# Optimization experiments

Measured on AMD Instinct MI355X. Metric: run time of the kernel, lower is better.

The kernel has to match this reference:

```python
import jax, jax.numpy as jnp
import numpy as np

B, S, EMB, H = 2, 2048, 1024, 16
D = EMB // H  # per-head dim = 64
SCALE = 1.0 / np.sqrt(D).astype(np.float32)


def setup_inputs() -> dict:
    key = jax.random.key(0)
    ks = jax.random.split(key, 11)
    lim = 1.0 / np.sqrt(EMB).astype(np.float32)  # torch Linear default init range
    def lin(kw, kb):
        W = jax.random.uniform(kw, (EMB, EMB), jnp.float32, -lim, lim)
        b = jax.random.uniform(kb, (EMB,), jnp.float32, -lim, lim)
        return W, b
    Wq, bq = lin(ks[0], ks[1])
    Wk, bk = lin(ks[2], ks[3])
    Wv, bv = lin(ks[4], ks[5])
    Wo, bo = lin(ks[6], ks[7])
    xq = jax.random.normal(ks[8], (B, S, EMB), jnp.float32)
    xk = jax.random.normal(ks[9], (B, S, EMB), jnp.float32)
    xv = jax.random.normal(ks[10], (B, S, EMB), jnp.float32)
    mask = jnp.tril(jnp.ones((S, S), dtype=jnp.int32))  # causal mask; 0 -> blocked
    return {"xq": xq, "xk": xk, "xv": xv, "mask": mask,
            "Wq": Wq, "bq": bq, "Wk": Wk, "bk": bk,
            "Wv": Wv, "bv": bv, "Wo": Wo, "bo": bo}


def reference(xq, xk, xv, mask, Wq, bq, Wk, bk, Wv, bv, Wo, bo):
    # Projections (torch Linear: x @ W.T + b), then split heads: [B,S,E] -> [B,H,S,D]
    def split_heads(x):
        return x.reshape(B, S, H, D).transpose(0, 2, 1, 3)
    Q = split_heads(xq @ Wq.T + bq)
    K = split_heads(xk @ Wk.T + bk)
    V = split_heads(xv @ Wv.T + bv)
    scores = jnp.einsum("bhqd,bhkd->bhqk", Q, K) * SCALE  # [B,H,S,S]
    scores = jnp.where(mask[None, None, :, :] == 0, jnp.float32(-1e9), scores)
    attn = jax.nn.softmax(scores, axis=-1)  # softmax over key axis (dim=2 per-head in torch)
    res = jnp.einsum("bhqk,bhkd->bhqd", attn, V)
    res = res.transpose(0, 2, 1, 3).reshape(B, S, EMB)  # merge heads back (same slicing layout)
    return res @ Wo.T + bo
```

## Files before the change

### kernel.cpp

```cpp
#include <hip/hip_runtime.h>
#include <hip/hip_bf16.h>

#define BB   2
#define SS   2048
#define EMBD 1024
#define NH   16
#define HD   64
#define SCALE 0.125f
#define NEG_BIG (-1e30f)

typedef __bf16 bf16;
typedef float  floatx4 __attribute__((ext_vector_type(4)));
typedef __bf16 bf16x4  __attribute__((ext_vector_type(4)));
typedef __bf16 bf16x8  __attribute__((ext_vector_type(8)));

typedef const __attribute__((address_space(1))) void* gas_ptr;
typedef __attribute__((address_space(3))) void*       las_ptr;

__device__ __forceinline__ void gl_lds16(const void* g, void* l) {
    __builtin_amdgcn_global_load_lds((gas_ptr)g, (las_ptr)l, 16, 0, 0);
}

__global__ __launch_bounds__(256) void cvt_all(
    const float* __restrict__ xq, const float* __restrict__ xk,
    const float* __restrict__ xv, const float* __restrict__ Wq,
    const float* __restrict__ Wk, const float* __restrict__ Wv,
    const float* __restrict__ Wo, bf16* __restrict__ xqo,
    bf16* __restrict__ xko, bf16* __restrict__ xvo, bf16* __restrict__ Wqo,
    bf16* __restrict__ Wko, bf16* __restrict__ Wvo, bf16* __restrict__ Woo) {
    const int y = blockIdx.y;
    const float* src;
    bf16* dst;
    size_t n;
    const size_t NX = (size_t)BB * SS * EMBD;
    const size_t NW = (size_t)EMBD * EMBD;
    switch (y) {
        case 0: src = xq; dst = xqo; n = NX; break;
        case 1: src = xk; dst = xko; n = NX; break;
        case 2: src = xv; dst = xvo; n = NX; break;
        case 3: src = Wq; dst = Wqo; n = NW; break;
        case 4: src = Wk; dst = Wko; n = NW; break;
        case 5: src = Wv; dst = Wvo; n = NW; break;
        default: src = Wo; dst = Woo; n = NW; break;
    }
    const size_t stride = (size_t)gridDim.x * blockDim.x * 4;
    for (size_t i = ((size_t)blockIdx.x * blockDim.x + threadIdx.x) * 4;
         i < n; i += stride) {
        floatx4 v = *(const floatx4*)(src + i);
        bf16x4 o = {(bf16)v[0], (bf16)v[1], (bf16)v[2], (bf16)v[3]};
        *(bf16x4*)(dst + i) = o;
    }
}

template <int MODE>
__device__ __forceinline__ void gemm_body(const bf16* __restrict__ A,
                                          const bf16* __restrict__ W,
                                          const float* __restrict__ bias,
                                          void* __restrict__ Ov,
                                          int mBase, int nBase) {
    __shared__ __align__(16) bf16 As[2 * 128 * 32];
    __shared__ __align__(16) bf16 Bs[2 * 128 * 32];

    const int t = threadIdx.x;
    const int l = t & 63, w = t >> 6;
    const int lm = l & 15, lq = l >> 4;
    const int K = 1024;
    const int wm = (w >> 1) * 64, wn = (w & 1) * 64;

    const floatx4 zero = {0.f, 0.f, 0.f, 0.f};
    floatx4 acc[4][4];
#pragma unroll
    for (int i = 0; i < 4; i++)
#pragma unroll
        for (int j = 0; j < 4; j++) acc[i][j] = zero;

    for (int kb = 0; kb < K; kb += 64) {
        __syncthreads();
#pragma unroll
        for (int i = 0; i < 4; i++) {
            int half = i >> 1;
            int rem  = (i & 1) * 256 + t;
            int row  = rem >> 2;
            int col  = half * 32 + (rem & 3) * 8;
            const bf16* ga = A + (size_t)(mBase + row) * K + kb + col;
            const bf16* gb = W + (size_t)(nBase + row) * K + kb + col;
            char* la = (char*)As + (i * 256 + w * 64) * 16;
            char* lb = (char*)Bs + (i * 256 + w * 64) * 16;
            gl_lds16(ga, la);
            gl_lds16(gb, lb);
        }
        __syncthreads();

#pragma unroll
        for (int half = 0; half < 2; half++) {
            const bf16* Ah = As + half * 128 * 32;
            const bf16* Bh = Bs + half * 128 * 32;
            bf16x8 af[4], bfv[4];
#pragma unroll
            for (int f = 0; f < 4; f++) {
                int rowA = wm + f * 16 + lm;
                af[f] = *(const bf16x8*)&Ah[rowA * 32 + lq * 8];
                int rowB = wn + f * 16 + lm;
                bfv[f] = *(const bf16x8*)&Bh[rowB * 32 + lq * 8];
            }
            if (MODE == 2) {
#pragma unroll
                for (int i = 0; i < 4; i++)
#pragma unroll
                    for (int j = 0; j < 4; j++)
                        acc[i][j] = __builtin_amdgcn_mfma_f32_16x16x32_bf16(
                            bfv[i], af[j], acc[i][j], 0, 0, 0);
            } else {
#pragma unroll
                for (int fm = 0; fm < 4; fm++)
#pragma unroll
                    for (int fn = 0; fn < 4; fn++)
                        acc[fm][fn] =
                            __builtin_amdgcn_mfma_f32_16x16x32_bf16(
                                af[fm], bfv[fn], acc[fm][fn], 0, 0, 0);
            }
        }
    }

    if (MODE == 2) {
#pragma unroll
        for (int i = 0; i < 4; i++)
#pragma unroll
            for (int j = 0; j < 4; j++) {
                int m = mBase + wm + j * 16 + lm;
                int b = m >> 11, s = m & 2047;
#pragma unroll
                for (int r = 0; r < 4; r++) {
                    int n = nBase + wn + i * 16 + lq * 4 + r;
                    int h = n >> 6, d = n & 63;
                    float v = acc[i][j][r] + bias[n];
                    ((bf16*)Ov)[((size_t)(b * NH + h) * HD + d) * SS + s] =
                        (bf16)v;
                }
            }
    } else {
#pragma unroll
        for (int fn = 0; fn < 4; fn++) {
            int n = nBase + wn + fn * 16 + lm;
            float bv = bias[n];
#pragma unroll
            for (int fm = 0; fm < 4; fm++) {
                int m0 = mBase + wm + fm * 16 + lq * 4;
#pragma unroll
                for (int r = 0; r < 4; r++) {
                    int m = m0 + r;
                    float v = acc[fm][fn][r] + bv;
                    if (MODE == 0) {
                        int b = m >> 11, s = m & 2047;
                        int h = n >> 6, d = n & 63;
                        ((bf16*)Ov)[(((size_t)(b * NH + h)) * SS + s) * HD +
                                    d] = (bf16)v;
                    } else {
                        ((float*)Ov)[(size_t)m * EMBD + n] = v;
                    }
                }
            }
        }
    }
}

__global__ __launch_bounds__(256, 2) void gemm_qkv(
    const bf16* __restrict__ xq, const bf16* __restrict__ xk,
    const bf16* __restrict__ xv, const bf16* __restrict__ Wq,
    const bf16* __restrict__ Wk, const bf16* __restrict__ Wv,
    const float* __restrict__ bq, const float* __restrict__ bk,
    const float* __restrict__ bv, bf16* __restrict__ Qo,
    bf16* __restrict__ Ko, bf16* __restrict__ Vo) {
    const int z = blockIdx.z;
    if (z == 0)
        gemm_body<0>(xq, Wq, bq, Qo, blockIdx.y * 128, blockIdx.x * 128);
    else if (z == 1)
        gemm_body<0>(xk, Wk, bk, Ko, blockIdx.y * 128, blockIdx.x * 128);
    else
        gemm_body<2>(xv, Wv, bv, Vo, blockIdx.y * 128, blockIdx.x * 128);
}

__global__ __launch_bounds__(256, 2) void gemm_out(
    const bf16* __restrict__ A, const bf16* __restrict__ W,
    const float* __restrict__ bias, float* __restrict__ O) {
    gemm_body<1>(A, W, bias, O, blockIdx.y * 128, blockIdx.x * 128);
}

__global__ __launch_bounds__(256, 2) void attn_fwd(
    const bf16* __restrict__ Qg, const bf16* __restrict__ Kg,
    const bf16* __restrict__ Vtg, bf16* __restrict__ Oatt) {
    __shared__ __align__(16) bf16 Ks[64 * 72];
    __shared__ __align__(16) bf16 VT[64 * 72];
    __shared__ __align__(16) bf16 Ps[4][16 * 72];

    const int t = threadIdx.x;
    const int l = t & 63, w = t >> 6;
    const int lm = l & 15, lq = l >> 4;
    const int bh = blockIdx.y;
    const size_t kbase = (size_t)bh * SS * HD;
    const size_t vbase = (size_t)bh * HD * SS;
    const int b = bh >> 4, h = bh & 15;
    const floatx4 zero = {0.f, 0.f, 0.f, 0.f};

#pragma unroll
    for (int job = 0; job < 2; ++job) {
        const int qt = job ? (31 - blockIdx.x) : blockIdx.x;

        bf16x8 qa0, qa1;
        {
            const bf16* qp =
                Qg + kbase + (size_t)(qt * 64 + w * 16 + lm) * HD + lq * 8;
            qa0 = *(const bf16x8*)qp;
            qa1 = *(const bf16x8*)(qp + 32);
        }

        float m_i = NEG_BIG, l_i = 0.f;
        floatx4 od[4];
#pragma unroll
        for (int dt = 0; dt < 4; dt++) od[dt] = zero;

        const int qglob = qt * 64 + w * 16 + lm;

        bf16x8 kreg[2], vreg[2];
#pragma unroll
        for (int i = 0; i < 2; i++) {
            int idx = i * 256 + t;
            int row = idx >> 3;
            int col = (idx & 7) * 8;
            kreg[i] = *(const bf16x8*)(Kg + kbase + (size_t)row * HD + col);
            vreg[i] = *(const bf16x8*)(Vtg + vbase + (size_t)row * SS + col);
        }

        for (int kt = 0; kt <= qt; ++kt) {
            __syncthreads();
#pragma unroll
            for (int i = 0; i < 2; i++) {
                int idx = i * 256 + t;
                int row = idx >> 3;
                int col = (idx & 7) * 8;
                *(bf16x8*)&Ks[row * 72 + col] = kreg[i];
                *(bf16x8*)&VT[row * 72 + col] = vreg[i];
            }
            __syncthreads();
            if (kt < qt) {
#pragma unroll
                for (int i = 0; i < 2; i++) {
                    int idx = i * 256 + t;
                    int row = idx >> 3;
                    int col = (idx & 7) * 8;
                    kreg[i] = *(const bf16x8*)(
                        Kg + kbase + (size_t)((kt + 1) * 64 + row) * HD + col);
                    vreg[i] = *(const bf16x8*)(
                        Vtg + vbase + (size_t)row * SS + (kt + 1) * 64 + col);
                }
            }

            floatx4 sc[4];
#pragma unroll
            for (int j0 = 0; j0 < 4; j0++) {
                int rowK = j0 * 16 + lm;
                bf16x8 k0 = *(const bf16x8*)&Ks[rowK * 72 + lq * 8];
                bf16x8 k1 = *(const bf16x8*)&Ks[rowK * 72 + 32 + lq * 8];
                floatx4 z = zero;
                z = __builtin_amdgcn_mfma_f32_16x16x32_bf16(k0, qa0, z, 0, 0,
                                                            0);
                z = __builtin_amdgcn_mfma_f32_16x16x32_bf16(k1, qa1, z, 0, 0,
                                                            0);
                sc[j0] = z;
            }
#pragma unroll
            for (int j0 = 0; j0 < 4; j0++)
#pragma unroll
                for (int r = 0; r < 4; r++) {
                    float v = sc[j0][r] * SCALE;
                    if (kt == qt) {
                        int key = kt * 64 + j0 * 16 + lq * 4 + r;
                        if (key > qglob) v = NEG_BIG;
                    }
                    sc[j0][r] = v;
                }
            float mt = sc[0][0];
#pragma unroll
            for (int j0 = 0; j0 < 4; j0++)
#pragma unroll
                for (int r = 0; r < 4; r++) mt = fmaxf(mt, sc[j0][r]);
            mt = fmaxf(mt, __shfl_xor(mt, 16));
            mt = fmaxf(mt, __shfl_xor(mt, 32));
            float mnew = fmaxf(m_i, mt);
            float alpha = __expf(m_i - mnew);
            m_i = mnew;
            float ps = 0.f;
#pragma unroll
            for (int j0 = 0; j0 < 4; j0++)
#pragma unroll
                for (int r = 0; r < 4; r++) {
                    float p = __expf(sc[j0][r] - mnew);
                    sc[j0][r] = p;
                    ps += p;
                }
            ps += __shfl_xor(ps, 16);
            ps += __shfl_xor(ps, 32);
            l_i = l_i * alpha + ps;
#pragma unroll
            for (int j0 = 0; j0 < 4; j0++) {
                bf16x4 pk = {(bf16)sc[j0][0], (bf16)sc[j0][1],
                             (bf16)sc[j0][2], (bf16)sc[j0][3]};
                *(bf16x4*)&Ps[w][lm * 72 + j0 * 16 + lq * 4] = pk;
            }
            float a0 = __shfl(alpha, lq * 4 + 0);
            float a1 = __shfl(alpha, lq * 4 + 1);
            float a2 = __shfl(alpha, lq * 4 + 2);
            float a3 = __shfl(alpha, lq * 4 + 3);
#pragma unroll
            for (int dt = 0; dt < 4; dt++) {
                od[dt][0] *= a0;
                od[dt][1] *= a1;
                od[dt][2] *= a2;
                od[dt][3] *= a3;
            }
            bf16x8 pa0 = *(const bf16x8*)&Ps[w][lm * 72 + lq * 8];
            bf16x8 pa1 = *(const bf16x8*)&Ps[w][lm * 72 + 32 + lq * 8];
#pragma unroll
            for (int dt = 0; dt < 4; dt++) {
                int rowD = dt * 16 + lm;
                bf16x8 v0 = *(const bf16x8*)&VT[rowD * 72 + lq * 8];
                bf16x8 v1 = *(const bf16x8*)&VT[rowD * 72 + 32 + lq * 8];
                od[dt] = __builtin_amdgcn_mfma_f32_16x16x32_bf16(pa0, v0,
                                                                 od[dt], 0, 0,
                                                                 0);
                od[dt] = __builtin_amdgcn_mfma_f32_16x16x32_bf16(pa1, v1,
                                                                 od[dt], 0, 0,
                                                                 0);
            }
        }

        float lr0 = __shfl(l_i, lq * 4 + 0);
        float lr1 = __shfl(l_i, lq * 4 + 1);
        float lr2 = __shfl(l_i, lq * 4 + 2);
        float lr3 = __shfl(l_i, lq * 4 + 3);
        float lr[4] = {lr0, lr1, lr2, lr3};
#pragma unroll
        for (int dt = 0; dt < 4; dt++) {
#pragma unroll
            for (int r = 0; r < 4; r++) {
                int s = qt * 64 + w * 16 + lq * 4 + r;
                float v = od[dt][r] / lr[r];
                Oatt[((size_t)(b * SS + s)) * EMBD + h * HD + dt * 16 + lm] =
                    (bf16)v;
            }
        }
    }
}

extern "C" void kernel_launch(void* const* d_in, const int* in_sizes, int n_in,
                              void* d_out, int out_size, void* d_ws,
                              size_t ws_size, hipStream_t stream) {
    const float* xq = (const float*)d_in[0];
    const float* xk = (const float*)d_in[1];
    const float* xv = (const float*)d_in[2];
    const float* Wq = (const float*)d_in[4];
    const float* bq = (const float*)d_in[5];
    const float* Wk = (const float*)d_in[6];
    const float* bk = (const float*)d_in[7];
    const float* Wv = (const float*)d_in[8];
    const float* bv = (const float*)d_in[9];
    const float* Wo = (const float*)d_in[10];
    const float* bo = (const float*)d_in[11];
    float* out = (float*)d_out;

    const size_t NX = (size_t)BB * SS * EMBD;
    const size_t NW = (size_t)EMBD * EMBD;
    bf16* Qw  = (bf16*)d_ws;
    bf16* Kw  = Qw + NX;
    bf16* Vw  = Kw + NX;
    bf16* Aw  = Vw + NX;
    bf16* xqb = Aw + NX;
    bf16* xkb = xqb + NX;
    bf16* xvb = xkb + NX;
    bf16* Wqb = xvb + NX;
    bf16* Wkb = Wqb + NW;
    bf16* Wvb = Wkb + NW;
    bf16* Wob = Wvb + NW;

    cvt_all<<<dim3(1024, 7), 256, 0, stream>>>(xq, xk, xv, Wq, Wk, Wv, Wo,
                                               xqb, xkb, xvb, Wqb, Wkb, Wvb,
                                               Wob);
    gemm_qkv<<<dim3(8, 32, 3), 256, 0, stream>>>(xqb, xkb, xvb, Wqb, Wkb, Wvb,
                                                 bq, bk, bv, Qw, Kw, Vw);
    attn_fwd<<<dim3(16, BB * NH), 256, 0, stream>>>(Qw, Kw, Vw, Aw);
    gemm_out<<<dim3(8, 32), 256, 0, stream>>>(Aw, Wob, bo, out);
}
```

Measured before the change: 240.2 us.

## Stage GEMM epilogues through LDS for vector stores and remap attention grid

The GEMM epilogues now write each wave's accumulator tile into shared memory and read it back so every lane can issue 16-byte stores. This replaces scattered 2-byte and 4-byte per-element global writes, which were worst for the transposed V output. The attention launch becomes a 1D grid of 512 blocks with a remapped (batch-head, q-tile) order, so blocks that share the same K/V head land near each other in the schedule for better cache locality. The cost is an extra LDS round trip and a barrier in the epilogue.

```diff
diff --git a/kernel.cpp b/kernel.cpp
--- a/kernel.cpp
+++ b/kernel.cpp
@@ -19,6 +19,13 @@
 
 __device__ __forceinline__ void gl_lds16(const void* g, void* l) {
     __builtin_amdgcn_global_load_lds((gas_ptr)g, (las_ptr)l, 16, 0, 0);
+}
+
+__device__ __forceinline__ bf16x8 cvt8(const float* p) {
+    bf16x8 o;
+#pragma unroll
+    for (int j = 0; j < 8; j++) o[j] = (bf16)p[j];
+    return o;
 }
 
 __global__ __launch_bounds__(256) void cvt_all(
@@ -58,8 +65,9 @@
                                           const float* __restrict__ bias,
                                           void* __restrict__ Ov,
                                           int mBase, int nBase) {
-    __shared__ __align__(16) bf16 As[2 * 128 * 32];
-    __shared__ __align__(16) bf16 Bs[2 * 128 * 32];
+    __shared__ __align__(16) char smem[32768];
+    bf16* As = (bf16*)smem;
+    bf16* Bs = (bf16*)(smem + 16384);
 
     const int t = threadIdx.x;
     const int l = t & 63, w = t >> 6;
@@ -122,43 +130,72 @@
         }
     }
 
-    if (MODE == 2) {
-#pragma unroll
-        for (int i = 0; i < 4; i++)
-#pragma unroll
-            for (int j = 0; j < 4; j++) {
-                int m = mBase + wm + j * 16 + lm;
-                int b = m >> 11, s = m & 2047;
-#pragma unroll
-                for (int r = 0; r < 4; r++) {
-                    int n = nBase + wn + i * 16 + lq * 4 + r;
-                    int h = n >> 6, d = n & 63;
-                    float v = acc[i][j][r] + bias[n];
-                    ((bf16*)Ov)[((size_t)(b * NH + h) * HD + d) * SS + s] =
-                        (bf16)v;
+    __syncthreads();
+    float* rp = (float*)smem + w * (16 * 68);
+
+    if (MODE != 2) {
+        float bvv[4];
+#pragma unroll
+        for (int fn = 0; fn < 4; fn++)
+            bvv[fn] = bias[nBase + wn + fn * 16 + lm];
+#pragma unroll
+        for (int fm = 0; fm < 4; fm++) {
+#pragma unroll
+            for (int fn = 0; fn < 4; fn++)
+#pragma unroll
+                for (int r = 0; r < 4; r++)
+                    rp[(lq * 4 + r) * 68 + fn * 16 + lm] =
+                        acc[fm][fn][r] + bvv[fn];
+            if (MODE == 0) {
+                int row2 = l >> 3, col8 = l & 7;
+                int h = (nBase + wn) >> 6;
+#pragma unroll
+                for (int p = 0; p < 2; p++) {
+                    int row = p * 8 + row2;
+                    int m = mBase + wm + fm * 16 + row;
+                    int b = m >> 11, s = m & 2047;
+                    bf16x8 o = cvt8(&rp[row * 68 + col8 * 8]);
+                    *(bf16x8*)((bf16*)Ov +
+                               (((size_t)(b * NH + h)) * SS + s) * HD +
+                               col8 * 8) = o;
                 }
-            }
+            } else {
+                int c4 = l & 15;
+#pragma unroll
+                for (int p = 0; p < 4; p++) {
+                    int row = p * 4 + (l >> 4);
+                    int m = mBase + wm + fm * 16 + row;
+                    floatx4 o = *(const floatx4*)&rp[row * 68 + c4 * 4];
+                    *(floatx4*)((float*)Ov + (size_t)m * EMBD + nBase + wn +
+                                c4 * 4) = o;
+                }
+            }
+        }
     } else {
-#pragma unroll
-        for (int fn = 0; fn < 4; fn++) {
-            int n = nBase + wn + fn * 16 + lm;
-            float bv = bias[n];
-#pragma unroll
-            for (int fm = 0; fm < 4; fm++) {
-                int m0 = mBase + wm + fm * 16 + lq * 4;
-#pragma unroll
-                for (int r = 0; r < 4; r++) {
-                    int m = m0 + r;
-                    float v = acc[fm][fn][r] + bv;
-                    if (MODE == 0) {
-                        int b = m >> 11, s = m & 2047;
-                        int h = n >> 6, d = n & 63;
-                        ((bf16*)Ov)[(((size_t)(b * NH + h)) * SS + s) * HD +
-                                    d] = (bf16)v;
-                    } else {
-                        ((float*)Ov)[(size_t)m * EMBD + n] = v;
-                    }
-                }
+        const int b = (mBase + wm) >> 11;
+        const int sbase = (mBase + wm) & 2047;
+#pragma unroll
+        for (int i = 0; i < 4; i++) {
+            float bv[4];
+#pragma unroll
+            for (int r = 0; r < 4; r++)
+                bv[r] = bias[nBase + wn + i * 16 + lq * 4 + r];
+#pragma unroll
+            for (int j = 0; j < 4; j++)
+#pragma unroll
+                for (int r = 0; r < 4; r++)
+                    rp[(lq * 4 + r) * 68 + j * 16 + lm] =
+                        acc[i][j][r] + bv[r];
+            int row2 = l >> 3, col8 = l & 7;
+#pragma unroll
+            for (int p = 0; p < 2; p++) {
+                int row = p * 8 + row2;
+                int n = nBase + wn + i * 16 + row;
+                int h = n >> 6, d = n & 63;
+                bf16x8 o = cvt8(&rp[row * 68 + col8 * 8]);
+                *(bf16x8*)((bf16*)Ov +
+                           ((size_t)(b * NH + h) * HD + d) * SS + sbase +
+                           col8 * 8) = o;
             }
         }
     }
@@ -196,7 +233,10 @@
     const int t = threadIdx.x;
     const int l = t & 63, w = t >> 6;
     const int lm = l & 15, lq = l >> 4;
-    const int bh = blockIdx.y;
+    const int x = blockIdx.x;
+    const int kk = x >> 3;
+    const int bh = ((kk & 3) << 3) | (x & 7);
+    const int qx = kk >> 2;
     const size_t kbase = (size_t)bh * SS * HD;
     const size_t vbase = (size_t)bh * HD * SS;
     const int b = bh >> 4, h = bh & 15;
@@ -204,7 +244,7 @@
 
 #pragma unroll
     for (int job = 0; job < 2; ++job) {
-        const int qt = job ? (31 - blockIdx.x) : blockIdx.x;
+        const int qt = job ? (31 - qx) : qx;
 
         bf16x8 qa0, qa1;
         {
@@ -387,6 +427,6 @@
                                                Wob);
     gemm_qkv<<<dim3(8, 32, 3), 256, 0, stream>>>(xqb, xkb, xvb, Wqb, Wkb, Wvb,
                                                  bq, bk, bv, Qw, Kw, Vw);
-    attn_fwd<<<dim3(16, BB * NH), 256, 0, stream>>>(Qw, Kw, Vw, Aw);
+    attn_fwd<<<dim3(512), 256, 0, stream>>>(Qw, Kw, Vw, Aw);
     gemm_out<<<dim3(8, 32), 256, 0, stream>>>(Aw, Wob, bo, out);
 }
```

Measured after the change: 240.6 us. About the same (+0.2%).
